# Optimization experiments

Hardware: AMD Instinct MI355X
Metric: run time of the kernel (lower is better)

## Reference

```python
import jax, jax.numpy as jnp
import numpy as np
import math

D_MODEL = 1024
N_HEADS = 16
D_HEAD = D_MODEL // N_HEADS


def _pos_encoding(seq_len, d_model):
    # matches get_pos_encoding: paired frequencies (repeat_interleave(2)),
    # sin on even columns, cos on odd columns of the SAME angle matrix.
    position = jnp.arange(seq_len, dtype=jnp.float32)[:, None]          # [L,1]
    div = 1.0 / (10000.0 ** (jnp.arange(0, d_model, 2, dtype=jnp.float32) / d_model))
    div = jnp.repeat(div, 2)[None, :]                                    # [1,D]
    ang = position * div                                                 # [L,D]
    col = jnp.arange(d_model)
    return jnp.where(col[None, :] % 2 == 0, jnp.sin(ang), jnp.cos(ang))


def _rel_enc_shift(a):
    # a: [b, h, l, m] -> Transformer-XL relative shift
    b, h, l, m = a.shape
    a = jnp.concatenate([a, jnp.zeros((b, h, l, 1), a.dtype)], axis=-1)  # [b,h,l,m+1]
    a = a.reshape(b, h, l * (m + 1))
    a = a[:, :, l - 1: l - 1 + l * m]
    return a.reshape(b, h, l, m)


def setup_inputs() -> dict:
    key = jax.random.key(0)
    ks = jax.random.split(key, 10)
    B, S, D = 1, 2048, D_MODEL
    s = 1.0 / math.sqrt(D)
    inp = {
        "query": jax.random.normal(ks[0], (B, S, D), jnp.float32),
        "key": jax.random.normal(ks[1], (B, S, D), jnp.float32),
        "value": jax.random.normal(ks[2], (B, S, D), jnp.float32),
        "attn_mask": jnp.zeros((1, 1, S, S), jnp.float32),
        "Wq": jax.random.normal(ks[3], (D, D), jnp.float32) * s,
        "Wke": jax.random.normal(ks[4], (D, D), jnp.float32) * s,
        "Wkr": jax.random.normal(ks[5], (D, D), jnp.float32) * s,
        "Wv": jax.random.normal(ks[6], (D, D), jnp.float32) * s,
        "Wf": jax.random.normal(ks[7], (D, D), jnp.float32) * s,
        "u_param": jax.random.normal(ks[8], (1, 1, N_HEADS, D_HEAD), jnp.float32),
        "v_param": jax.random.normal(ks[9], (1, 1, N_HEADS, D_HEAD), jnp.float32),
    }
    return inp


def reference(query, key, value, attn_mask, Wq, Wke, Wkr, Wv, Wf, u_param, v_param):
    B, S, D = query.shape
    F = key.shape[1]
    H, dh = u_param.shape[2], u_param.shape[3]
    sqrt_dk = math.sqrt(D)

    rel_enc = _pos_encoding(F, D)[::-1, :]                     # flipped along seq dim

    q = (query @ Wq.T).reshape(B, S, H, dh)
    k = (key @ Wke.T).reshape(B, F, H, dh)
    v = (value @ Wv.T).reshape(B, F, H, dh)

    A_C = jnp.einsum('bsnd,bfnd->bnsf', q + u_param, k)
    Q = (rel_enc @ Wkr.T).reshape(F, H, dh)
    B_D_hat = jnp.einsum('bsnd,fnd->bnsf', q + v_param, Q)
    B_D = _rel_enc_shift(B_D_hat)

    score = (A_C + B_D) / sqrt_dk + attn_mask
    weights = jax.nn.softmax(score, axis=-1)                   # [B,H,S,F]
    attention_loss = jnp.mean(jnp.max(weights, axis=(-1, -2)))

    out = jnp.einsum('bnsf,bfnd->bsnd', weights, v).reshape(B, S, D)
    out = jax.nn.gelu(out @ Wf.T, approximate=False)
    return out, weights, attention_loss
```

## Files before the change

### kernel.cpp

```cpp
#include <hip/hip_runtime.h>
#include <math.h>

#define SEQ 2048
#define DMODEL 1024
#define NHEADS 16
#define DHEAD 64

#define LSLOTS 64
#define LSTRIDE 32

typedef long long i64;
typedef unsigned short u16;
typedef __attribute__((ext_vector_type(4))) float f32x4;
typedef __attribute__((ext_vector_type(8))) short bf16x8;

#define IN_E  2097152
#define W_E   1048576
#define HEAD_E 131072

__device__ inline u16 f2bf(float x) {
    union { float f; unsigned u; } v; v.f = x;
    unsigned r = v.u + 0x7FFF + ((v.u >> 16) & 1);
    return (u16)(r >> 16);
}
__device__ inline float bf2f(u16 h) {
    union { unsigned u; float f; } v; v.u = ((unsigned)h) << 16;
    return v.f;
}

__device__ inline void gload16(const void* g, void* l) {
    __builtin_amdgcn_global_load_lds(
        (const __attribute__((address_space(1))) unsigned int*)g,
        (__attribute__((address_space(3))) unsigned int*)l, 16, 0, 0);
}

struct SplitArgs {
    const float* src[8];
    u16* dh[8];
    u16* dl[8];
    int n4[8];
};
__global__ __launch_bounds__(256)
void split_all(SplitArgs a)
{
    const int z = blockIdx.y;
    const int i = blockIdx.x * 256 + threadIdx.x;
    if (i >= a.n4[z]) return;
    const float4 x = ((const float4*)a.src[z])[i];
    u16 h0 = f2bf(x.x), h1 = f2bf(x.y), h2 = f2bf(x.z), h3 = f2bf(x.w);
    u16 l0 = f2bf(x.x - bf2f(h0)), l1 = f2bf(x.y - bf2f(h1));
    u16 l2 = f2bf(x.z - bf2f(h2)), l3 = f2bf(x.w - bf2f(h3));
    uint2 hh; hh.x = (unsigned)h0 | ((unsigned)h1 << 16); hh.y = (unsigned)h2 | ((unsigned)h3 << 16);
    uint2 ll; ll.x = (unsigned)l0 | ((unsigned)l1 << 16); ll.y = (unsigned)l2 | ((unsigned)l3 << 16);
    ((uint2*)a.dh[z])[i] = hh;
    ((uint2*)a.dl[z])[i] = ll;
}

__global__ __launch_bounds__(256)
void posenc_split(u16* __restrict__ dh, u16* __restrict__ dl)
{
    const int idx = blockIdx.x * 256 + threadIdx.x;
    const int f = idx >> 10;
    const int i = idx & 1023;
    const float P = (float)(SEQ - 1 - f);
    const float ex = (float)(i & ~1) * (1.f / 1024.f);
    const float dv = __expf(ex * -9.210340372f);
    const float ang = P * dv;
    const float val = (i & 1) ? __cosf(ang) : __sinf(ang);
    const u16 hb = f2bf(val);
    dh[idx] = hb;
    dl[idx] = f2bf(val - bf2f(hb));
}

struct TNArgs {
    const u16 *Ah, *Al, *Bh, *Bl;
    i64 sAz, sBz;
    float* Cf; i64 sCz; int ldc;
    u16 *O1h, *O1l, *O2h, *O2l;
    const float *b1, *b2;
    int K, mode;
};

__global__ __launch_bounds__(256)
void mfma_tn128(TNArgs p)
{
    __shared__ __align__(16) u16 Ash[128 * 32];
    __shared__ __align__(16) u16 Asl[128 * 32];
    __shared__ __align__(16) u16 Bsh[128 * 32];
    __shared__ __align__(16) u16 Bsl[128 * 32];
    const int tid = threadIdx.x, wave = tid >> 6, lane = tid & 63;
    const int z = blockIdx.z;
    const i64 m0 = (i64)blockIdx.y * 128, n0 = (i64)blockIdx.x * 128;
    const int K = p.K;
    const u16* Abh = p.Ah + (i64)z * p.sAz;
    const u16* Abl = p.Al + (i64)z * p.sAz;
    const u16* Bbh = p.Bh + (i64)z * p.sBz;
    const u16* Bbl = p.Bl + (i64)z * p.sBz;
    const int r0 = tid >> 2, kc = (tid & 3) * 8;
    const int r1 = r0 + 64;
    u16* dA0 = &Ash[wave * 512];
    u16* dA1 = &Ash[2048 + wave * 512];
    u16* dA0l = &Asl[wave * 512];
    u16* dA1l = &Asl[2048 + wave * 512];
    u16* dB0 = &Bsh[wave * 512];
    u16* dB1 = &Bsh[2048 + wave * 512];
    u16* dB0l = &Bsl[wave * 512];
    u16* dB1l = &Bsl[2048 + wave * 512];
    const int wm = (wave >> 1) * 64, wn = (wave & 1) * 64;
    f32x4 acc[4][4] = {};

    for (int k0 = 0; k0 < K; k0 += 32) {
        __syncthreads();
        const i64 ga0 = (m0 + r0) * K + k0 + kc;
        const i64 ga1 = (m0 + r1) * K + k0 + kc;
        const i64 gb0 = (n0 + r0) * K + k0 + kc;
        const i64 gb1 = (n0 + r1) * K + k0 + kc;
        gload16(Abh + ga0, dA0);  gload16(Abh + ga1, dA1);
        gload16(Abl + ga0, dA0l); gload16(Abl + ga1, dA1l);
        gload16(Bbh + gb0, dB0);  gload16(Bbh + gb1, dB1);
        gload16(Bbl + gb0, dB0l); gload16(Bbl + gb1, dB1l);
        __syncthreads();
        const int fr = lane & 15, fk = (lane >> 4) * 8;
        bf16x8 fah[4], fal[4], fbh[4], fbl[4];
#pragma unroll
        for (int t = 0; t < 4; ++t) {
            fah[t] = *(const bf16x8*)&Ash[(wm + t * 16 + fr) * 32 + fk];
            fal[t] = *(const bf16x8*)&Asl[(wm + t * 16 + fr) * 32 + fk];
            fbh[t] = *(const bf16x8*)&Bsh[(wn + t * 16 + fr) * 32 + fk];
            fbl[t] = *(const bf16x8*)&Bsl[(wn + t * 16 + fr) * 32 + fk];
        }
#pragma unroll
        for (int mi = 0; mi < 4; ++mi)
#pragma unroll
            for (int ni = 0; ni < 4; ++ni) {
                acc[mi][ni] = __builtin_amdgcn_mfma_f32_16x16x32_bf16(fah[mi], fbh[ni], acc[mi][ni], 0, 0, 0);
                acc[mi][ni] = __builtin_amdgcn_mfma_f32_16x16x32_bf16(fah[mi], fbl[ni], acc[mi][ni], 0, 0, 0);
                acc[mi][ni] = __builtin_amdgcn_mfma_f32_16x16x32_bf16(fal[mi], fbh[ni], acc[mi][ni], 0, 0, 0);
            }
    }

    const int fr = lane & 15, fq = (lane >> 4) * 4;
    if (p.mode == 0) {
        float* C = p.Cf + (i64)z * p.sCz;
#pragma unroll
        for (int mi = 0; mi < 4; ++mi)
#pragma unroll
            for (int e = 0; e < 4; ++e) {
                const i64 row = m0 + wm + mi * 16 + fq + e;
#pragma unroll
                for (int ni = 0; ni < 4; ++ni)
                    C[row * p.ldc + n0 + wn + ni * 16 + fr] = acc[mi][ni][e];
            }
    } else if (p.mode == 1) {
        const i64 obase = (i64)z * IN_E;
#pragma unroll
        for (int mi = 0; mi < 4; ++mi)
#pragma unroll
            for (int e = 0; e < 4; ++e) {
                const i64 m = m0 + wm + mi * 16 + fq + e;
#pragma unroll
                for (int ni = 0; ni < 4; ++ni) {
                    const int c = (int)n0 + wn + ni * 16 + fr;
                    const int h = c >> 6, d = c & 63;
                    const i64 off = ((i64)h * SEQ + m) * DHEAD + d;
                    float v = acc[mi][ni][e];
                    if (z == 0) v += p.b1[c];
                    const u16 hb = f2bf(v);
                    const u16 lb = f2bf(v - bf2f(hb));
                    p.O1h[obase + off] = hb;
                    p.O1l[obase + off] = lb;
                    if (z == 0) {
                        const float v2 = acc[mi][ni][e] + p.b2[c];
                        const u16 hb2 = f2bf(v2);
                        const u16 lb2 = f2bf(v2 - bf2f(hb2));
                        p.O2h[off] = hb2;
                        p.O2l[off] = lb2;
                    }
                }
            }
    } else {
        float* C = p.Cf;
#pragma unroll
        for (int mi = 0; mi < 4; ++mi)
#pragma unroll
            for (int e = 0; e < 4; ++e) {
                const i64 row = m0 + wm + mi * 16 + fq + e;
#pragma unroll
                for (int ni = 0; ni < 4; ++ni) {
                    const float x = acc[mi][ni][e];
                    C[row * p.ldc + n0 + wn + ni * 16 + fr] =
                        0.5f * x * (1.f + erff(x * 0.70710678118654752f));
                }
            }
    }
}

__global__ __launch_bounds__(256)
void mfma_pv(const float* __restrict__ Wgt, const u16* __restrict__ VTh,
             const u16* __restrict__ VTl, u16* __restrict__ Oh, u16* __restrict__ Ol)
{
    __shared__ __align__(16) float Asf[64 * 32];
    __shared__ __align__(16) u16 Bsh[64 * 32];
    __shared__ __align__(16) u16 Bsl[64 * 32];
    const int tid = threadIdx.x, wave = tid >> 6, lane = tid & 63;
    const int z = blockIdx.z;
    const i64 m0 = (i64)blockIdx.y * 64;
    const float* A = Wgt + (i64)z * SEQ * SEQ;
    const u16* Bh = VTh + (i64)z * HEAD_E;
    const u16* Bl = VTl + (i64)z * HEAD_E;
    const int ar = tid >> 3, akc = (tid & 7) * 4;
    const int br = tid >> 2, bkc = (tid & 3) * 8;
    const int wm = wave * 16;
    f32x4 acc[4] = {};

    for (int k0 = 0; k0 < SEQ; k0 += 32) {
        __syncthreads();
#pragma unroll
        for (int i = 0; i < 2; ++i)
            gload16(A + (m0 + ar + i * 32) * SEQ + k0 + akc, &Asf[(i * 256 + wave * 64) * 4]);
        gload16(Bh + (i64)br * SEQ + k0 + bkc, &Bsh[wave * 512]);
        gload16(Bl + (i64)br * SEQ + k0 + bkc, &Bsl[wave * 512]);
        __syncthreads();
        const int fr = lane & 15, fk = (lane >> 4) * 8;
        bf16x8 fbh[4], fbl[4];
#pragma unroll
        for (int t = 0; t < 4; ++t) {
            fbh[t] = *(const bf16x8*)&Bsh[(t * 16 + fr) * 32 + fk];
            fbl[t] = *(const bf16x8*)&Bsl[(t * 16 + fr) * 32 + fk];
        }
        const float4 x0 = *(const float4*)&Asf[(wm + fr) * 32 + fk];
        const float4 x1 = *(const float4*)&Asf[(wm + fr) * 32 + fk + 4];
        float av[8] = { x0.x, x0.y, x0.z, x0.w, x1.x, x1.y, x1.z, x1.w };
        bf16x8 ah, al;
#pragma unroll
        for (int j = 0; j < 8; ++j) {
            union { float f; unsigned u; } v; v.f = av[j];
            const u16 hb = (u16)(v.u >> 16);
            union { unsigned u; float f; } fh; fh.u = v.u & 0xFFFF0000u;
            union { float f; unsigned u; } rm; rm.f = av[j] - fh.f;
            ah[j] = (short)hb;
            al[j] = (short)(u16)(rm.u >> 16);
        }
#pragma unroll
        for (int ni = 0; ni < 4; ++ni) {
            acc[ni] = __builtin_amdgcn_mfma_f32_16x16x32_bf16(ah, fbh[ni], acc[ni], 0, 0, 0);
            acc[ni] = __builtin_amdgcn_mfma_f32_16x16x32_bf16(ah, fbl[ni], acc[ni], 0, 0, 0);
            acc[ni] = __builtin_amdgcn_mfma_f32_16x16x32_bf16(al, fbh[ni], acc[ni], 0, 0, 0);
        }
    }

    const int fr = lane & 15, fq = (lane >> 4) * 4;
#pragma unroll
    for (int e = 0; e < 4; ++e) {
        const i64 m = m0 + wm + fq + e;
#pragma unroll
        for (int ni = 0; ni < 4; ++ni) {
            const int c = z * 64 + ni * 16 + fr;
            const float v = acc[ni][e];
            const u16 hb = f2bf(v);
            Oh[m * DMODEL + c] = hb;
            Ol[m * DMODEL + c] = f2bf(v - bf2f(hb));
        }
    }
}

__global__ __launch_bounds__(256)
void transpose_vv(const u16* __restrict__ vh, const u16* __restrict__ vl,
                  u16* __restrict__ th, u16* __restrict__ tl)
{
    __shared__ u16 tile[64][65];
    const int tid = threadIdx.x;
    const int h = blockIdx.y, f0 = blockIdx.x * 64;
    const i64 src = ((i64)h * SEQ + f0) * DHEAD;
    const i64 dst = (i64)h * HEAD_E + f0;
#pragma unroll
    for (int i = 0; i < 16; ++i) {
        const int idx = i * 256 + tid;
        const int r = idx >> 6, c = idx & 63;
        tile[c][r] = vh[src + (i64)r * 64 + c];
    }
    __syncthreads();
#pragma unroll
    for (int i = 0; i < 16; ++i) {
        const int idx = i * 256 + tid;
        const int d = idx >> 6, fl = idx & 63;
        th[dst + (i64)d * SEQ + fl] = tile[d][fl];
    }
    __syncthreads();
#pragma unroll
    for (int i = 0; i < 16; ++i) {
        const int idx = i * 256 + tid;
        const int r = idx >> 6, c = idx & 63;
        tile[c][r] = vl[src + (i64)r * 64 + c];
    }
    __syncthreads();
#pragma unroll
    for (int i = 0; i < 16; ++i) {
        const int idx = i * 256 + tid;
        const int d = idx >> 6, fl = idx & 63;
        tl[dst + (i64)d * SEQ + fl] = tile[d][fl];
    }
}

__global__ __launch_bounds__(256)
void softmax_rows(float* __restrict__ Wbase, const float* __restrict__ Gbase,
                  const float* __restrict__ mask, unsigned int* __restrict__ lmin, int h0)
{
    __shared__ float red[4];
    const int hl = blockIdx.y;
    float* Wh = Wbase + (i64)(h0 + hl) * SEQ * SEQ;
    const float* G = Gbase + (i64)hl * SEQ * SEQ;
    const int i = blockIdx.x;
    const int tx = threadIdx.x;
    const i64 rowoff = (i64)i * SEQ;
    float s[8];
    float mloc = -3.0e38f;
#pragma unroll
    for (int r = 0; r < 8; ++r) {
        const int j = tx + (r << 8);
        float bd;
        if (j <= i)          bd = G[rowoff + (SEQ - 1 - i + j)];
        else if (j == i + 1) bd = 0.f;
        else                 bd = G[rowoff + SEQ + (j - i - 2)];
        const float v = (Wh[rowoff + j] + bd) * 0.03125f + mask[rowoff + j];
        s[r] = v;
        mloc = fmaxf(mloc, v);
    }
#pragma unroll
    for (int o = 32; o > 0; o >>= 1) mloc = fmaxf(mloc, __shfl_xor(mloc, o));
    if ((tx & 63) == 0) red[tx >> 6] = mloc;
    __syncthreads();
    const float m = fmaxf(fmaxf(red[0], red[1]), fmaxf(red[2], red[3]));
    __syncthreads();
    float lsum = 0.f;
#pragma unroll
    for (int r = 0; r < 8; ++r) { s[r] = __expf(s[r] - m); lsum += s[r]; }
#pragma unroll
    for (int o = 32; o > 0; o >>= 1) lsum += __shfl_xor(lsum, o);
    if ((tx & 63) == 0) red[tx >> 6] = lsum;
    __syncthreads();
    const float l = red[0] + red[1] + red[2] + red[3];
    const float inv = 1.f / l;
#pragma unroll
    for (int r = 0; r < 8; ++r) Wh[rowoff + tx + (r << 8)] = s[r] * inv;
    if (tx == 0)
        atomicMin(&lmin[(((h0 + hl) << 6) + (i & (LSLOTS - 1))) * LSTRIDE],
                  __float_as_uint(l));
}

__global__ __launch_bounds__(1024)
void init_kernel(unsigned int* __restrict__ lmin)
{
    lmin[threadIdx.x * LSTRIDE] = 0x7F7FFFFFu;
}

__global__ __launch_bounds__(1024)
void loss_kernel(const unsigned int* __restrict__ lmin, float* __restrict__ out)
{
    __shared__ float hs[16];
    const int w = threadIdx.x >> 6;
    const int lane = threadIdx.x & 63;
    float l = __uint_as_float(lmin[threadIdx.x * LSTRIDE]);
#pragma unroll
    for (int o = 32; o > 0; o >>= 1) l = fminf(l, __shfl_xor(l, o));
    if (lane == 0) hs[w] = 1.f / l;
    __syncthreads();
    if (threadIdx.x == 0) {
        float v = 0.f;
#pragma unroll
        for (int h = 0; h < 16; ++h) v += hs[h];
        *out = v * (1.f / NHEADS);
    }
}

extern "C" void kernel_launch(void* const* d_in, const int* in_sizes, int n_in,
                              void* d_out, int out_size, void* d_ws, size_t ws_size,
                              hipStream_t stream)
{
    const float* query = (const float*)d_in[0];
    const float* key   = (const float*)d_in[1];
    const float* value = (const float*)d_in[2];
    const float* mask  = (const float*)d_in[3];
    const float* Wq    = (const float*)d_in[4];
    const float* Wke   = (const float*)d_in[5];
    const float* Wkr   = (const float*)d_in[6];
    const float* Wv    = (const float*)d_in[7];
    const float* Wf    = (const float*)d_in[8];
    const float* u_p   = (const float*)d_in[9];
    const float* v_p   = (const float*)d_in[10];

    float* out_final = (float*)d_out;
    float* weights   = out_final + (i64)SEQ * DMODEL;
    float* loss      = weights + (i64)NHEADS * SEQ * SEQ;

    char* w = (char*)d_ws;
    u16* in_h = (u16*)w;               w += (i64)4 * IN_E * 2;
    u16* in_l = (u16*)w;               w += (i64)4 * IN_E * 2;
    u16* W_h  = (u16*)w;               w += (i64)5 * W_E * 2;
    u16* W_l  = (u16*)w;               w += (i64)5 * W_E * 2;
    u16* P_h  = (u16*)w;               w += (i64)4 * IN_E * 2;
    u16* P_l  = (u16*)w;               w += (i64)4 * IN_E * 2;
    u16* qv_h = (u16*)w;               w += (i64)IN_E * 2;
    u16* qv_l = (u16*)w;               w += (i64)IN_E * 2;
    u16* vvT_h = (u16*)w;              w += (i64)IN_E * 2;
    u16* vvT_l = (u16*)w;              w += (i64)IN_E * 2;
    u16* o_h  = (u16*)w;               w += (i64)IN_E * 2;
    u16* o_l  = (u16*)w;               w += (i64)IN_E * 2;
    unsigned int* lmin = (unsigned int*)w; w += (i64)NHEADS * LSLOTS * LSTRIDE * 4;
    const i64 fixed_bytes = (i64)(w - (char*)d_ws);
    const i64 gbytes = (i64)SEQ * SEQ * 4;
    const i64 avail = (i64)ws_size - fixed_bytes;
    float* G;
    int chunk;
    if (avail >= gbytes) {
        G = (float*)w;
        i64 ch = avail / gbytes;
        chunk = ch > 16 ? 16 : (int)ch;
    } else {
        G = (float*)in_h;
        chunk = 2;
    }

    dim3 blk(256);
    init_kernel<<<dim3(1), dim3(1024), 0, stream>>>(lmin);

    SplitArgs sa;
    sa.src[0] = query; sa.dh[0] = in_h;           sa.dl[0] = in_l;           sa.n4[0] = IN_E / 4;
    sa.src[1] = key;   sa.dh[1] = in_h + IN_E;    sa.dl[1] = in_l + IN_E;    sa.n4[1] = IN_E / 4;
    sa.src[2] = value; sa.dh[2] = in_h + 2*IN_E;  sa.dl[2] = in_l + 2*IN_E;  sa.n4[2] = IN_E / 4;
    sa.src[3] = Wq;    sa.dh[3] = W_h;            sa.dl[3] = W_l;            sa.n4[3] = W_E / 4;
    sa.src[4] = Wke;   sa.dh[4] = W_h + W_E;      sa.dl[4] = W_l + W_E;      sa.n4[4] = W_E / 4;
    sa.src[5] = Wv;    sa.dh[5] = W_h + 2*W_E;    sa.dl[5] = W_l + 2*W_E;    sa.n4[5] = W_E / 4;
    sa.src[6] = Wkr;   sa.dh[6] = W_h + 3*W_E;    sa.dl[6] = W_l + 3*W_E;    sa.n4[6] = W_E / 4;
    sa.src[7] = Wf;    sa.dh[7] = W_h + 4*W_E;    sa.dl[7] = W_l + 4*W_E;    sa.n4[7] = W_E / 4;
    split_all<<<dim3(2048, 8), blk, 0, stream>>>(sa);
    posenc_split<<<dim3(IN_E / 256), blk, 0, stream>>>(in_h + 3*(i64)IN_E, in_l + 3*(i64)IN_E);

    {
        TNArgs p = {};
        p.Ah = in_h; p.Al = in_l; p.Bh = W_h; p.Bl = W_l;
        p.sAz = IN_E; p.sBz = W_E;
        p.O1h = P_h; p.O1l = P_l; p.O2h = qv_h; p.O2l = qv_l;
        p.b1 = u_p; p.b2 = v_p;
        p.K = DMODEL; p.mode = 1;
        mfma_tn128<<<dim3(DMODEL / 128, SEQ / 128, 4), blk, 0, stream>>>(p);
    }

    transpose_vv<<<dim3(SEQ / 64, NHEADS), blk, 0, stream>>>(
        P_h + 2*(i64)IN_E, P_l + 2*(i64)IN_E, vvT_h, vvT_l);

    {
        TNArgs p = {};
        p.Ah = P_h; p.Al = P_l;
        p.Bh = P_h + IN_E; p.Bl = P_l + IN_E;
        p.sAz = HEAD_E; p.sBz = HEAD_E;
        p.Cf = weights; p.sCz = (i64)SEQ * SEQ; p.ldc = SEQ;
        p.K = DHEAD; p.mode = 0;
        mfma_tn128<<<dim3(SEQ / 128, SEQ / 128, NHEADS), blk, 0, stream>>>(p);
    }

    for (int h0 = 0; h0 < NHEADS; h0 += chunk) {
        const int ch = (h0 + chunk <= NHEADS) ? chunk : (NHEADS - h0);
        TNArgs p = {};
        p.Ah = qv_h + (i64)h0 * HEAD_E; p.Al = qv_l + (i64)h0 * HEAD_E;
        p.Bh = P_h + 3*(i64)IN_E + (i64)h0 * HEAD_E;
        p.Bl = P_l + 3*(i64)IN_E + (i64)h0 * HEAD_E;
        p.sAz = HEAD_E; p.sBz = HEAD_E;
        p.Cf = G; p.sCz = (i64)SEQ * SEQ; p.ldc = SEQ;
        p.K = DHEAD; p.mode = 0;
        mfma_tn128<<<dim3(SEQ / 128, SEQ / 128, ch), blk, 0, stream>>>(p);
        softmax_rows<<<dim3(SEQ, ch), blk, 0, stream>>>(weights, G, mask, lmin, h0);
    }

    mfma_pv<<<dim3(1, SEQ / 64, NHEADS), blk, 0, stream>>>(weights, vvT_h, vvT_l, o_h, o_l);

    {
        TNArgs p = {};
        p.Ah = o_h; p.Al = o_l;
        p.Bh = W_h + 4*(i64)W_E; p.Bl = W_l + 4*(i64)W_E;
        p.sAz = 0; p.sBz = 0;
        p.Cf = out_final; p.sCz = 0; p.ldc = DMODEL;
        p.K = DMODEL; p.mode = 2;
        mfma_tn128<<<dim3(DMODEL / 128, SEQ / 128, 1), blk, 0, stream>>>(p);
    }

    loss_kernel<<<dim3(1), dim3(1024), 0, stream>>>(lmin, loss);
}
```

Measured before the change: 568.8 us.

## Fuse content-score QK^T GEMM into softmax kernel, drop weights round-trip

Removes the separate A_C GEMM that wrote full fp32 scores into the weights buffer. A new kernel computes a 16-row by 2048-column block of A_C per workgroup with split-bf16 MFMA into a large shared-memory tile. It then applies the shifted B_D, mask and softmax, writing the weights once. This saves one full write and one full read of the 16x2048x2048 fp32 score tensor, at the cost of 1024-thread blocks limited to one per CU by about 131KB of LDS, and per-element scalar gathers of G.

```diff
diff --git a/kernel.cpp b/kernel.cpp
--- a/kernel.cpp
+++ b/kernel.cpp
@@ -195,6 +195,98 @@
     }
 }
 
+__global__ __launch_bounds__(1024, 1)
+void ac_softmax(const u16* __restrict__ QUh, const u16* __restrict__ QUl,
+                const u16* __restrict__ KKh, const u16* __restrict__ KKl,
+                const float* __restrict__ Gbase, const float* __restrict__ mask,
+                float* __restrict__ Wbase, unsigned int* __restrict__ lmin, int h0)
+{
+    __shared__ __align__(16) float S[16][2052];
+    const int tid = threadIdx.x, wave = tid >> 6, lane = tid & 63;
+    const int hl = blockIdx.y;
+    const int h = h0 + hl;
+    const int r0 = blockIdx.x * 16;
+    const i64 hb = (i64)h * HEAD_E;
+    const int n = lane & 15;
+    const int kc8 = (lane >> 4) * 8;
+
+    bf16x8 qa[2][2];
+    {
+        const i64 mo = hb + (i64)(r0 + n) * 64 + kc8;
+#pragma unroll
+        for (int ks = 0; ks < 2; ++ks) {
+            qa[ks][0] = *(const bf16x8*)&QUh[mo + ks * 32];
+            qa[ks][1] = *(const bf16x8*)&QUl[mo + ks * 32];
+        }
+    }
+
+    for (int t = wave; t < 128; t += 16) {
+        const int ft = t * 16;
+        const i64 ao = hb + (i64)(ft + n) * 64 + kc8;
+        const bf16x8 a0h = *(const bf16x8*)&KKh[ao];
+        const bf16x8 a0l = *(const bf16x8*)&KKl[ao];
+        const bf16x8 a1h = *(const bf16x8*)&KKh[ao + 32];
+        const bf16x8 a1l = *(const bf16x8*)&KKl[ao + 32];
+        f32x4 a = {};
+        a = __builtin_amdgcn_mfma_f32_16x16x32_bf16(a0h, qa[0][0], a, 0, 0, 0);
+        a = __builtin_amdgcn_mfma_f32_16x16x32_bf16(a0h, qa[0][1], a, 0, 0, 0);
+        a = __builtin_amdgcn_mfma_f32_16x16x32_bf16(a0l, qa[0][0], a, 0, 0, 0);
+        a = __builtin_amdgcn_mfma_f32_16x16x32_bf16(a1h, qa[1][0], a, 0, 0, 0);
+        a = __builtin_amdgcn_mfma_f32_16x16x32_bf16(a1h, qa[1][1], a, 0, 0, 0);
+        a = __builtin_amdgcn_mfma_f32_16x16x32_bf16(a1l, qa[1][0], a, 0, 0, 0);
+        const int fb = ft + (lane >> 4) * 4;
+        *(f32x4*)&S[n][fb] = a;
+    }
+    __syncthreads();
+
+    const int lr = wave;
+    const int i = r0 + lr;
+    const float* G = Gbase + (i64)hl * SEQ * SEQ;
+    const i64 rowoff = (i64)i * SEQ;
+    float sv[32];
+    float mloc = -3.0e38f;
+#pragma unroll
+    for (int q = 0; q < 8; ++q) {
+        const int j0 = q * 256 + lane * 4;
+        const f32x4 ac = *(const f32x4*)&S[lr][j0];
+        const float4 mk = *(const float4*)&mask[rowoff + j0];
+        const float m4[4] = { mk.x, mk.y, mk.z, mk.w };
+#pragma unroll
+        for (int e = 0; e < 4; ++e) {
+            const int j = j0 + e;
+            float bd;
+            if (j <= i)          bd = G[rowoff + (SEQ - 1 - i + j)];
+            else if (j == i + 1) bd = 0.f;
+            else                 bd = G[rowoff + SEQ + (j - i - 2)];
+            const float v = (ac[e] + bd) * 0.03125f + m4[e];
+            sv[q * 4 + e] = v;
+            mloc = fmaxf(mloc, v);
+        }
+    }
+#pragma unroll
+    for (int o = 32; o > 0; o >>= 1) mloc = fmaxf(mloc, __shfl_xor(mloc, o));
+    float lsum = 0.f;
+#pragma unroll
+    for (int q = 0; q < 32; ++q) { sv[q] = __expf(sv[q] - mloc); lsum += sv[q]; }
+#pragma unroll
+    for (int o = 32; o > 0; o >>= 1) lsum += __shfl_xor(lsum, o);
+    const float inv = 1.f / lsum;
+    float* Wh = Wbase + (i64)h * SEQ * SEQ;
+#pragma unroll
+    for (int q = 0; q < 8; ++q) {
+        const int j0 = q * 256 + lane * 4;
+        float4 ov;
+        ov.x = sv[q * 4 + 0] * inv;
+        ov.y = sv[q * 4 + 1] * inv;
+        ov.z = sv[q * 4 + 2] * inv;
+        ov.w = sv[q * 4 + 3] * inv;
+        *(float4*)&Wh[rowoff + j0] = ov;
+    }
+    if (lane == 0)
+        atomicMin(&lmin[(((unsigned)h << 6) + (i & (LSLOTS - 1))) * LSTRIDE],
+                  __float_as_uint(lsum));
+}
+
 __global__ __launch_bounds__(256)
 void mfma_pv(const float* __restrict__ Wgt, const u16* __restrict__ VTh,
              const u16* __restrict__ VTl, u16* __restrict__ Oh, u16* __restrict__ Ol)
@@ -300,52 +392,6 @@
         const int d = idx >> 6, fl = idx & 63;
         tl[dst + (i64)d * SEQ + fl] = tile[d][fl];
     }
-}
-
-__global__ __launch_bounds__(256)
-void softmax_rows(float* __restrict__ Wbase, const float* __restrict__ Gbase,
-                  const float* __restrict__ mask, unsigned int* __restrict__ lmin, int h0)
-{
-    __shared__ float red[4];
-    const int hl = blockIdx.y;
-    float* Wh = Wbase + (i64)(h0 + hl) * SEQ * SEQ;
-    const float* G = Gbase + (i64)hl * SEQ * SEQ;
-    const int i = blockIdx.x;
-    const int tx = threadIdx.x;
-    const i64 rowoff = (i64)i * SEQ;
-    float s[8];
-    float mloc = -3.0e38f;
-#pragma unroll
-    for (int r = 0; r < 8; ++r) {
-        const int j = tx + (r << 8);
-        float bd;
-        if (j <= i)          bd = G[rowoff + (SEQ - 1 - i + j)];
-        else if (j == i + 1) bd = 0.f;
-        else                 bd = G[rowoff + SEQ + (j - i - 2)];
-        const float v = (Wh[rowoff + j] + bd) * 0.03125f + mask[rowoff + j];
-        s[r] = v;
-        mloc = fmaxf(mloc, v);
-    }
-#pragma unroll
-    for (int o = 32; o > 0; o >>= 1) mloc = fmaxf(mloc, __shfl_xor(mloc, o));
-    if ((tx & 63) == 0) red[tx >> 6] = mloc;
-    __syncthreads();
-    const float m = fmaxf(fmaxf(red[0], red[1]), fmaxf(red[2], red[3]));
-    __syncthreads();
-    float lsum = 0.f;
-#pragma unroll
-    for (int r = 0; r < 8; ++r) { s[r] = __expf(s[r] - m); lsum += s[r]; }
-#pragma unroll
-    for (int o = 32; o > 0; o >>= 1) lsum += __shfl_xor(lsum, o);
-    if ((tx & 63) == 0) red[tx >> 6] = lsum;
-    __syncthreads();
-    const float l = red[0] + red[1] + red[2] + red[3];
-    const float inv = 1.f / l;
-#pragma unroll
-    for (int r = 0; r < 8; ++r) Wh[rowoff + tx + (r << 8)] = s[r] * inv;
-    if (tx == 0)
-        atomicMin(&lmin[(((h0 + hl) << 6) + (i & (LSLOTS - 1))) * LSTRIDE],
-                  __float_as_uint(l));
 }
 
 __global__ __launch_bounds__(1024)
@@ -449,27 +495,22 @@
     transpose_vv<<<dim3(SEQ / 64, NHEADS), blk, 0, stream>>>(
         P_h + 2*(i64)IN_E, P_l + 2*(i64)IN_E, vvT_h, vvT_l);
 
-    {
-        TNArgs p = {};
-        p.Ah = P_h; p.Al = P_l;
-        p.Bh = P_h + IN_E; p.Bl = P_l + IN_E;
-        p.sAz = HEAD_E; p.sBz = HEAD_E;
-        p.Cf = weights; p.sCz = (i64)SEQ * SEQ; p.ldc = SEQ;
-        p.K = DHEAD; p.mode = 0;
-        mfma_tn128<<<dim3(SEQ / 128, SEQ / 128, NHEADS), blk, 0, stream>>>(p);
-    }
-
     for (int h0 = 0; h0 < NHEADS; h0 += chunk) {
         const int ch = (h0 + chunk <= NHEADS) ? chunk : (NHEADS - h0);
-        TNArgs p = {};
-        p.Ah = qv_h + (i64)h0 * HEAD_E; p.Al = qv_l + (i64)h0 * HEAD_E;
-        p.Bh = P_h + 3*(i64)IN_E + (i64)h0 * HEAD_E;
-        p.Bl = P_l + 3*(i64)IN_E + (i64)h0 * HEAD_E;
-        p.sAz = HEAD_E; p.sBz = HEAD_E;
-        p.Cf = G; p.sCz = (i64)SEQ * SEQ; p.ldc = SEQ;
-        p.K = DHEAD; p.mode = 0;
-        mfma_tn128<<<dim3(SEQ / 128, SEQ / 128, ch), blk, 0, stream>>>(p);
-        softmax_rows<<<dim3(SEQ, ch), blk, 0, stream>>>(weights, G, mask, lmin, h0);
+        {
+            TNArgs p = {};
+            p.Ah = qv_h + (i64)h0 * HEAD_E; p.Al = qv_l + (i64)h0 * HEAD_E;
+            p.Bh = P_h + 3*(i64)IN_E + (i64)h0 * HEAD_E;
+            p.Bl = P_l + 3*(i64)IN_E + (i64)h0 * HEAD_E;
+            p.sAz = HEAD_E; p.sBz = HEAD_E;
+            p.Cf = G; p.sCz = (i64)SEQ * SEQ; p.ldc = SEQ;
+            p.K = DHEAD; p.mode = 0;
+            mfma_tn128<<<dim3(SEQ / 128, SEQ / 128, ch), blk, 0, stream>>>(p);
+        }
+        ac_softmax<<<dim3(SEQ / 16, ch), dim3(1024), 0, stream>>>(
+            P_h, P_l,
+            P_h + IN_E, P_l + IN_E,
+            G, mask, weights, lmin, h0);
     }
 
     mfma_pv<<<dim3(1, SEQ / 64, NHEADS), blk, 0, stream>>>(weights, vvT_h, vvT_l, o_h, o_l);
```

New measurement: 587.6 us. 1.03x slower.
